# Optimization experiments

Hardware: AMD Instinct MI355X
Metric: run time of the kernel (lower is better)

## Reference

```python
import jax, jax.numpy as jnp
import numpy as np

B, T, D = 2, 2048, 1024
NH = 16
HD = D // NH


def setup_inputs() -> dict:
    key = jax.random.key(0)
    ks = jax.random.split(key, 5)
    s = 0.02
    return {
        "x": jax.random.normal(ks[0], (B, T, D), dtype=jnp.float32),
        "Wq": jax.random.normal(ks[1], (D, D), dtype=jnp.float32) * s,
        "Wk": jax.random.normal(ks[2], (D, D), dtype=jnp.float32) * s,
        "Wv": jax.random.normal(ks[3], (D, D), dtype=jnp.float32) * s,
        "Wo": jax.random.normal(ks[4], (D, D), dtype=jnp.float32) * s,
        "bo": jnp.zeros((D,), dtype=jnp.float32),
    }


def reference(x, Wq, Wk, Wv, Wo, bo):
    b, t, _ = x.shape
    scale = HD ** -0.5
    # torch Linear: y = x @ W^T
    q = (x @ Wq.T).reshape(b, t, NH, HD)
    k = (x @ Wk.T).reshape(b, t, NH, HD)
    v = (x @ Wv.T).reshape(b, t, NH, HD)
    # scores: [b, nh, t, t]
    s = jnp.einsum("bqhd,bkhd->bhqk", q, k) * scale
    causal = jnp.tril(jnp.ones((t, t), dtype=bool))
    s = jnp.where(causal, s, -jnp.inf)
    p = jax.nn.softmax(s, axis=-1)
    o = jnp.einsum("bhqk,bkhd->bqhd", p, v).reshape(b, t, D)
    return o @ Wo.T + bo
```

## Files before the change

kernel.cpp:

```cpp
#include <hip/hip_runtime.h>


typedef __bf16 bf16x8 __attribute__((ext_vector_type(8)));
typedef float f32x4 __attribute__((ext_vector_type(4)));
typedef unsigned short ushortx8 __attribute__((ext_vector_type(8)));
typedef unsigned short ushortx4 __attribute__((ext_vector_type(4)));

#define T_SEQ 2048
#define NHEAD 16
#define HDIM 64
#define DMODEL 1024

__device__ inline unsigned short f2bf(float f) {
  unsigned int u = __builtin_bit_cast(unsigned int, f);
  unsigned int r = (u + 0x7fffu + ((u >> 16) & 1u)) >> 16;
  return (unsigned short)r;
}

__device__ inline void gl16(const unsigned short* g, unsigned short* l) {
  __builtin_amdgcn_global_load_lds(
      (const __attribute__((address_space(1))) unsigned int*)g,
      (__attribute__((address_space(3))) unsigned int*)l, 16, 0, 0);
}

__global__ void cast_all(const float* __restrict__ x, const float* __restrict__ w0,
                         const float* __restrict__ w1, const float* __restrict__ w2,
                         const float* __restrict__ w3, unsigned short* __restrict__ out) {
  const int NX = 2 * T_SEQ * DMODEL;
  int i = (blockIdx.x * 256 + threadIdx.x) * 4;
  const float* src;
  int off;
  if (i < NX) {
    src = x; off = i;
  } else {
    const int j = i - NX;
    const int sel = j >> 20;
    off = j & ((1 << 20) - 1);
    src = sel == 0 ? w0 : sel == 1 ? w1 : sel == 2 ? w2 : w3;
  }
  float4 v = *reinterpret_cast<const float4*>(src + off);
  ushortx4 o;
  o[0] = f2bf(v.x); o[1] = f2bf(v.y); o[2] = f2bf(v.z); o[3] = f2bf(v.w);
  *reinterpret_cast<ushortx4*>(out + i) = o;
}

__device__ __forceinline__ void gemm_core(
    const unsigned short* __restrict__ A, const unsigned short* __restrict__ Bw,
    int K, int m0, int n0, f32x4 acc[4][4]) {
  __shared__ unsigned short As[4096];
  __shared__ unsigned short Bs[4096];
  const int tid = threadIdx.x;
  const int lane = tid & 63, wid = tid >> 6;
  const int wr = wid >> 1, wc = wid & 1;
  const int lr = lane & 15, lg = lane >> 4;
  const int srow = tid >> 2;
  const int scs = ((tid & 3) ^ (srow & 3)) * 8;
  const unsigned short* ga0 = A + (size_t)(m0 + srow) * K + scs;
  const unsigned short* gb0 = Bw + (size_t)(n0 + srow) * K + scs;
  unsigned short* la0 = As + tid * 8;
  unsigned short* lb0 = Bs + tid * 8;
  const int rca = (lg ^ (lr & 3)) * 8;

  for (int k0 = 0; k0 < K; k0 += 32) {
    __syncthreads();
    gl16(ga0 + k0, la0);
    gl16(ga0 + (size_t)64 * K + k0, la0 + 2048);
    gl16(gb0 + k0, lb0);
    gl16(gb0 + (size_t)64 * K + k0, lb0 + 2048);
    __syncthreads();

    bf16x8 af[4], bfr[4];
#pragma unroll
    for (int t = 0; t < 4; ++t) {
      af[t]  = *reinterpret_cast<const bf16x8*>(&As[(wr * 64 + t * 16 + lr) * 32 + rca]);
      bfr[t] = *reinterpret_cast<const bf16x8*>(&Bs[(wc * 64 + t * 16 + lr) * 32 + rca]);
    }
#pragma unroll
    for (int mi = 0; mi < 4; ++mi)
#pragma unroll
      for (int ni = 0; ni < 4; ++ni)
        acc[mi][ni] = __builtin_amdgcn_mfma_f32_16x16x32_bf16(af[mi], bfr[ni], acc[mi][ni], 0, 0, 0);
  }
}

__global__ __launch_bounds__(256) void gemm_qkv(
    const unsigned short* __restrict__ xb, const unsigned short* __restrict__ Wall,
    unsigned short* __restrict__ Qb, unsigned short* __restrict__ Kb,
    unsigned short* __restrict__ Vtb) {
  const int z = blockIdx.y;
  const int bid = blockIdx.x;
  int m0, n0;
  const unsigned short* A;
  const unsigned short* Bw;
  if (z < 2) {
    n0 = (bid & 7) * 128; m0 = (bid >> 3) * 128;
    A = xb; Bw = Wall + (size_t)z * (DMODEL * DMODEL);
  } else {
    m0 = (bid & 7) * 128; n0 = (bid >> 3) * 128;
    A = Wall + (size_t)2 * (DMODEL * DMODEL); Bw = xb;
  }
  f32x4 acc[4][4] = {};
  gemm_core(A, Bw, DMODEL, m0, n0, acc);

  const int tid = threadIdx.x, lane = tid & 63, wid = tid >> 6;
  const int wr = wid >> 1, wc = wid & 1, lr = lane & 15, lg = lane >> 4;
  const int mb = m0 + wr * 64, nb = n0 + wc * 64;
  const float scale = z == 0 ? 0.125f * 1.44269504089f : 1.0f;
#pragma unroll
  for (int mi = 0; mi < 4; ++mi)
#pragma unroll
    for (int ni = 0; ni < 4; ++ni) {
      const int col = nb + ni * 16 + lr;
#pragma unroll
      for (int j = 0; j < 4; ++j) {
        const int row = mb + mi * 16 + lg * 4 + j;
        const float v = acc[mi][ni][j] * scale;
        if (z < 2) {
          const int b = row >> 11, t = row & (T_SEQ - 1);
          const int h = col >> 6, d = col & (HDIM - 1);
          unsigned short* out = z == 0 ? Qb : Kb;
          out[(((size_t)(b * NHEAD + h) * T_SEQ + t) << 6) + d] = f2bf(v);
        } else {
          const int h = row >> 6, d = row & (HDIM - 1);
          const int b = col >> 11, t = col & (T_SEQ - 1);
          Vtb[(((size_t)(b * NHEAD + h) * HDIM + d) << 11) + t] = f2bf(v);
        }
      }
    }
}

__global__ __launch_bounds__(256) void gemm_proj(
    const unsigned short* __restrict__ Ob, const unsigned short* __restrict__ Wob,
    float* __restrict__ out, const float* __restrict__ bias) {
  const int m0 = blockIdx.y * 128, n0 = blockIdx.x * 128;
  f32x4 acc[4][4] = {};
  gemm_core(Ob, Wob, DMODEL, m0, n0, acc);

  const int tid = threadIdx.x, lane = tid & 63, wid = tid >> 6;
  const int wr = wid >> 1, wc = wid & 1, lr = lane & 15, lg = lane >> 4;
  const int mb = m0 + wr * 64, nb = n0 + wc * 64;
#pragma unroll
  for (int mi = 0; mi < 4; ++mi)
#pragma unroll
    for (int ni = 0; ni < 4; ++ni) {
      const int col = nb + ni * 16 + lr;
      const float bv = bias[col];
#pragma unroll
      for (int j = 0; j < 4; ++j) {
        const int row = mb + mi * 16 + lg * 4 + j;
        out[(size_t)row * DMODEL + col] = acc[mi][ni][j] + bv;
      }
    }
}

__global__ __launch_bounds__(256, 4) void flash_attn(
    const unsigned short* __restrict__ Q, const unsigned short* __restrict__ Kg,
    const unsigned short* __restrict__ Vt, unsigned short* __restrict__ O) {
  __shared__ unsigned short Ks[3][4096];
  __shared__ unsigned short Vs[3][4096];
  const int tid = threadIdx.x, lane = tid & 63, wid = tid >> 6;
  const int lr = lane & 15, lg = lane >> 4;
  const int bid = blockIdx.x;
  const int bh = (bid & 7) * 4 + ((bid >> 3) & 3);
  const int qt = 31 - (bid >> 5);
  const int qg = qt * 64 + wid * 16;
  const size_t base = (size_t)bh * (T_SEQ * HDIM);
  const int q = qg + lr;

  bf16x8 qf[2];
#pragma unroll
  for (int h = 0; h < 2; ++h)
    qf[h] = *reinterpret_cast<const bf16x8*>(Q + base + (size_t)(qg + lr) * HDIM + h * 32 + lg * 8);
  asm volatile("s_waitcnt vmcnt(0)" ::: "memory");

  const int srow = tid >> 3;
  const int schk = ((tid & 7) ^ (srow & 7)) * 8;
  const unsigned short* kst = Kg + base + (size_t)srow * HDIM + schk;
  const unsigned short* vst = Vt + base + (size_t)srow * T_SEQ + schk;

#define STAGE(buf, kt_)                                              \
  do {                                                               \
    const int kb_ = (kt_) * 64;                                      \
    gl16(kst + (size_t)kb_ * HDIM, &Ks[buf][tid * 8]);               \
    gl16(kst + (size_t)(kb_ + 32) * HDIM, &Ks[buf][2048 + tid * 8]); \
    gl16(vst + kb_, &Vs[buf][tid * 8]);                              \
    gl16(vst + 32 * T_SEQ + kb_, &Vs[buf][2048 + tid * 8]);          \
  } while (0)

  int koff[4][2];
#pragma unroll
  for (int c = 0; c < 4; ++c)
#pragma unroll
    for (int h = 0; h < 2; ++h)
      koff[c][h] = (c * 16 + lr) * 64 + (((h * 4 + lg) ^ (lr & 7)) * 8);
  int voff[4][2][2];
#pragma unroll
  for (int dt = 0; dt < 4; ++dt)
#pragma unroll
    for (int ks = 0; ks < 2; ++ks) {
      const int g0 = (ks * 4 + (lg >> 1)) ^ (lr & 7);
      const int g1 = (ks * 4 + 2 + (lg >> 1)) ^ (lr & 7);
      voff[dt][ks][0] = (dt * 16 + lr) * 64 + g0 * 8 + (lg & 1) * 4;
      voff[dt][ks][1] = (dt * 16 + lr) * 64 + g1 * 8 + (lg & 1) * 4;
    }

  float mrun = -INFINITY, lrun = 0.f;
  f32x4 acc[4] = {};
  const int nt = qt + 1;

  STAGE(0, 0);
  STAGE(1, 1);
  int cb = 0;

  for (int kt = 0; kt < nt; ++kt) {
    const int ahead = qt - kt;
    if (ahead >= 2) {
      int nb2 = cb + 2; if (nb2 >= 3) nb2 -= 3;
      STAGE(nb2, kt + 2);
      asm volatile("s_waitcnt vmcnt(8)" ::: "memory");
    } else if (ahead == 1) {
      asm volatile("s_waitcnt vmcnt(4)" ::: "memory");
    } else {
      asm volatile("s_waitcnt vmcnt(0)" ::: "memory");
    }
    __builtin_amdgcn_s_barrier();
    asm volatile("" ::: "memory");

    const int kb = kt * 64;
    f32x4 s[4] = {};
    bf16x8 kf[4][2];
#pragma unroll
    for (int c = 0; c < 4; ++c)
#pragma unroll
      for (int h = 0; h < 2; ++h)
        kf[c][h] = *reinterpret_cast<const bf16x8*>(&Ks[cb][koff[c][h]]);
    __builtin_amdgcn_s_setprio(1);
#pragma unroll
    for (int c = 0; c < 4; ++c)
#pragma unroll
      for (int h = 0; h < 2; ++h)
        s[c] = __builtin_amdgcn_mfma_f32_16x16x32_bf16(kf[c][h], qf[h], s[c], 0, 0, 0);
    __builtin_amdgcn_s_setprio(0);

    if (kt == qt) {
#pragma unroll
      for (int c = 0; c < 4; ++c)
#pragma unroll
        for (int j = 0; j < 4; ++j) {
          const int k = kb + c * 16 + lg * 4 + j;
          if (k > q) s[c][j] = -INFINITY;
        }
    }
    float tm = -INFINITY;
#pragma unroll
    for (int c = 0; c < 4; ++c)
#pragma unroll
      for (int j = 0; j < 4; ++j) tm = fmaxf(tm, s[c][j]);
    tm = fmaxf(tm, __shfl_xor(tm, 16, 64));
    tm = fmaxf(tm, __shfl_xor(tm, 32, 64));
    if (!__all(tm <= mrun + 8.f)) {
      const float mnew = fmaxf(mrun, tm);
      const float fac = exp2f(mrun - mnew);
      lrun *= fac;
#pragma unroll
      for (int dt = 0; dt < 4; ++dt)
#pragma unroll
        for (int j = 0; j < 4; ++j) acc[dt][j] *= fac;
      mrun = mnew;
    }
    float tsum = 0.f;
#pragma unroll
    for (int c = 0; c < 4; ++c)
#pragma unroll
      for (int j = 0; j < 4; ++j) {
        const float p = exp2f(s[c][j] - mrun);
        s[c][j] = p;
        tsum += p;
      }
    tsum += __shfl_xor(tsum, 16, 64);
    tsum += __shfl_xor(tsum, 32, 64);
    lrun += tsum;

    bf16x8 pb[2];
#pragma unroll
    for (int ks = 0; ks < 2; ++ks) {
      bf16x8 t8;
#pragma unroll
      for (int e = 0; e < 8; ++e) t8[e] = (__bf16)s[ks * 2 + (e >> 2)][e & 3];
      pb[ks] = t8;
    }
    __builtin_amdgcn_s_setprio(1);
#pragma unroll
    for (int dt = 0; dt < 4; ++dt) {
#pragma unroll
      for (int ks = 0; ks < 2; ++ks) {
        uint2 vlo = *reinterpret_cast<const uint2*>(&Vs[cb][voff[dt][ks][0]]);
        uint2 vhi = *reinterpret_cast<const uint2*>(&Vs[cb][voff[dt][ks][1]]);
        uint4 u;
        u.x = vlo.x; u.y = vlo.y; u.z = vhi.x; u.w = vhi.y;
        bf16x8 vf = __builtin_bit_cast(bf16x8, u);
        acc[dt] = __builtin_amdgcn_mfma_f32_16x16x32_bf16(vf, pb[ks], acc[dt], 0, 0, 0);
      }
    }
    __builtin_amdgcn_s_setprio(0);

    asm volatile("" ::: "memory");
    __builtin_amdgcn_s_barrier();
    ++cb; if (cb >= 3) cb -= 3;
  }
#undef STAGE

  const int b = bh >> 4, h = bh & (NHEAD - 1);
  const float inv = 1.0f / lrun;
  unsigned short* orow = O + (((size_t)(b * T_SEQ + q)) << 10) + h * HDIM + lg * 4;
#pragma unroll
  for (int dt = 0; dt < 4; ++dt) {
    ushortx4 o4;
#pragma unroll
    for (int j = 0; j < 4; ++j) o4[j] = f2bf(acc[dt][j] * inv);
    *reinterpret_cast<ushortx4*>(orow + dt * 16) = o4;
  }
}

extern "C" void kernel_launch(void* const* d_in, const int* in_sizes, int n_in,
                              void* d_out, int out_size, void* d_ws, size_t ws_size,
                              hipStream_t stream) {
  const float* x  = (const float*)d_in[0];
  const float* Wq = (const float*)d_in[1];
  const float* Wk = (const float*)d_in[2];
  const float* Wv = (const float*)d_in[3];
  const float* Wo = (const float*)d_in[4];
  const float* bo = (const float*)d_in[5];
  float* out = (float*)d_out;

  const int M = 2 * T_SEQ;
  const int NXD = DMODEL * DMODEL;
  const int NX = M * DMODEL;

  unsigned short* ws = (unsigned short*)d_ws;
  unsigned short* xb  = ws;
  unsigned short* Wqb = xb + NX;
  unsigned short* Wob = Wqb + 3 * (size_t)NXD;
  unsigned short* Qb  = Wqb + 4 * (size_t)NXD;
  unsigned short* Kbf = Qb + NX;
  unsigned short* Vtb = Kbf + NX;
  unsigned short* Ob  = Vtb + NX;

  cast_all<<<(NX + 4 * NXD) / 1024, 256, 0, stream>>>(x, Wq, Wk, Wv, Wo, xb);

  dim3 gq(256, 3);
  gemm_qkv<<<gq, 256, 0, stream>>>(xb, Wqb, Qb, Kbf, Vtb);

  flash_attn<<<1024, 256, 0, stream>>>(Qb, Kbf, Vtb, Ob);

  dim3 gg(DMODEL / 128, M / 128);
  gemm_proj<<<gg, 256, 0, stream>>>(Ob, Wob, out, bo);
}
```

Before: 117.8 us.

## Load K directly into registers and double-buffer V in LDS

K tiles are no longer staged through LDS. Each wave loads its K fragments straight from global memory into registers, prefetching the next tile into a second register set. V drops from a 3-deep to a 2-deep LDS ring with a single barrier per iteration, and the launch-bounds occupancy hint falls from 4 to 3. This removes the K LDS traffic and shrinks shared memory, but raises register pressure and makes every wave fetch K from global memory itself, with less prefetch depth.

```diff
diff --git a/kernel.cpp b/kernel.cpp
--- a/kernel.cpp
+++ b/kernel.cpp
@@ -153,11 +153,10 @@
     }
 }
 
-__global__ __launch_bounds__(256, 4) void flash_attn(
+__global__ __launch_bounds__(256, 3) void flash_attn(
     const unsigned short* __restrict__ Q, const unsigned short* __restrict__ Kg,
     const unsigned short* __restrict__ Vt, unsigned short* __restrict__ O) {
-  __shared__ unsigned short Ks[3][4096];
-  __shared__ unsigned short Vs[3][4096];
+  __shared__ unsigned short Vs[2][4096];
   const int tid = threadIdx.x, lane = tid & 63, wid = tid >> 6;
   const int lr = lane & 15, lg = lane >> 4;
   const int bid = blockIdx.x;
@@ -171,28 +170,27 @@
 #pragma unroll
   for (int h = 0; h < 2; ++h)
     qf[h] = *reinterpret_cast<const bf16x8*>(Q + base + (size_t)(qg + lr) * HDIM + h * 32 + lg * 8);
-  asm volatile("s_waitcnt vmcnt(0)" ::: "memory");
 
   const int srow = tid >> 3;
   const int schk = ((tid & 7) ^ (srow & 7)) * 8;
-  const unsigned short* kst = Kg + base + (size_t)srow * HDIM + schk;
   const unsigned short* vst = Vt + base + (size_t)srow * T_SEQ + schk;
 
-#define STAGE(buf, kt_)                                              \
-  do {                                                               \
-    const int kb_ = (kt_) * 64;                                      \
-    gl16(kst + (size_t)kb_ * HDIM, &Ks[buf][tid * 8]);               \
-    gl16(kst + (size_t)(kb_ + 32) * HDIM, &Ks[buf][2048 + tid * 8]); \
-    gl16(vst + kb_, &Vs[buf][tid * 8]);                              \
-    gl16(vst + 32 * T_SEQ + kb_, &Vs[buf][2048 + tid * 8]);          \
+#define STAGE(buf, kt_)                                      \
+  do {                                                       \
+    const int kb_ = (kt_) * 64;                              \
+    gl16(vst + kb_, &Vs[buf][tid * 8]);                      \
+    gl16(vst + 32 * T_SEQ + kb_, &Vs[buf][2048 + tid * 8]);  \
   } while (0)
 
-  int koff[4][2];
-#pragma unroll
-  for (int c = 0; c < 4; ++c)
-#pragma unroll
-    for (int h = 0; h < 2; ++h)
-      koff[c][h] = (c * 16 + lr) * 64 + (((h * 4 + lg) ^ (lr & 7)) * 8);
+  const unsigned short* kp = Kg + base + (size_t)lr * HDIM + lg * 8;
+#define KLOAD(dst, kt_)                                                      \
+  do {                                                                       \
+    const unsigned short* kpp = kp + (size_t)(kt_) * 64 * HDIM;              \
+    _Pragma("unroll") for (int c = 0; c < 4; ++c)                            \
+      _Pragma("unroll") for (int h = 0; h < 2; ++h)                          \
+        dst[c][h] = *reinterpret_cast<const bf16x8*>(kpp + c * 16 * HDIM + h * 32); \
+  } while (0)
+
   int voff[4][2][2];
 #pragma unroll
   for (int dt = 0; dt < 4; ++dt)
@@ -208,38 +206,27 @@
   f32x4 acc[4] = {};
   const int nt = qt + 1;
 
+  bf16x8 kfA[4][2], kfB[4][2];
   STAGE(0, 0);
-  STAGE(1, 1);
-  int cb = 0;
+  KLOAD(kfA, 0);
 
   for (int kt = 0; kt < nt; ++kt) {
-    const int ahead = qt - kt;
-    if (ahead >= 2) {
-      int nb2 = cb + 2; if (nb2 >= 3) nb2 -= 3;
-      STAGE(nb2, kt + 2);
-      asm volatile("s_waitcnt vmcnt(8)" ::: "memory");
-    } else if (ahead == 1) {
-      asm volatile("s_waitcnt vmcnt(4)" ::: "memory");
-    } else {
-      asm volatile("s_waitcnt vmcnt(0)" ::: "memory");
-    }
+    asm volatile("s_waitcnt vmcnt(0)" ::: "memory");
     __builtin_amdgcn_s_barrier();
     asm volatile("" ::: "memory");
+    if (kt + 1 < nt) {
+      STAGE((kt + 1) & 1, kt + 1);
+      KLOAD(kfB, kt + 1);
+    }
 
     const int kb = kt * 64;
     f32x4 s[4] = {};
-    bf16x8 kf[4][2];
+    __builtin_amdgcn_s_setprio(1);
 #pragma unroll
     for (int c = 0; c < 4; ++c)
 #pragma unroll
       for (int h = 0; h < 2; ++h)
-        kf[c][h] = *reinterpret_cast<const bf16x8*>(&Ks[cb][koff[c][h]]);
-    __builtin_amdgcn_s_setprio(1);
-#pragma unroll
-    for (int c = 0; c < 4; ++c)
-#pragma unroll
-      for (int h = 0; h < 2; ++h)
-        s[c] = __builtin_amdgcn_mfma_f32_16x16x32_bf16(kf[c][h], qf[h], s[c], 0, 0, 0);
+        s[c] = __builtin_amdgcn_mfma_f32_16x16x32_bf16(kfA[c][h], qf[h], s[c], 0, 0, 0);
     __builtin_amdgcn_s_setprio(0);
 
     if (kt == qt) {
@@ -294,8 +281,8 @@
     for (int dt = 0; dt < 4; ++dt) {
 #pragma unroll
       for (int ks = 0; ks < 2; ++ks) {
-        uint2 vlo = *reinterpret_cast<const uint2*>(&Vs[cb][voff[dt][ks][0]]);
-        uint2 vhi = *reinterpret_cast<const uint2*>(&Vs[cb][voff[dt][ks][1]]);
+        uint2 vlo = *reinterpret_cast<const uint2*>(&Vs[kt & 1][voff[dt][ks][0]]);
+        uint2 vhi = *reinterpret_cast<const uint2*>(&Vs[kt & 1][voff[dt][ks][1]]);
         uint4 u;
         u.x = vlo.x; u.y = vlo.y; u.z = vhi.x; u.w = vhi.y;
         bf16x8 vf = __builtin_bit_cast(bf16x8, u);
@@ -304,11 +291,15 @@
     }
     __builtin_amdgcn_s_setprio(0);
 
-    asm volatile("" ::: "memory");
-    __builtin_amdgcn_s_barrier();
-    ++cb; if (cb >= 3) cb -= 3;
+    if (kt + 1 < nt) {
+#pragma unroll
+      for (int c = 0; c < 4; ++c)
+#pragma unroll
+        for (int h = 0; h < 2; ++h) kfA[c][h] = kfB[c][h];
+    }
   }
 #undef STAGE
+#undef KLOAD
 
   const int b = bh >> 4, h = bh & (NHEAD - 1);
   const float inv = 1.0f / lrun;
```

After: 150.1 us. 27.4% more time.

## Double-buffer GEMM LDS tiles and switch attention to two-stage prefetch

Applied to the files above, without the earlier changes.

The GEMM core now holds two LDS buffers and prefetches the next K tile while MFMAs run on the current one. Before, each K step had a full load-and-wait between two barriers. The flash attention kernel goes from a three-buffer, two-ahead pipeline to a two-buffer, one-ahead scheme with one vmcnt(0)+barrier per iteration. This cuts LDS use and may raise occupancy, but leaves less time to hide load latency in attention. The GEMM also doubles its LDS footprint.

```diff
diff --git a/kernel.cpp b/kernel.cpp
--- a/kernel.cpp
+++ b/kernel.cpp
@@ -47,8 +47,8 @@
 __device__ __forceinline__ void gemm_core(
     const unsigned short* __restrict__ A, const unsigned short* __restrict__ Bw,
     int K, int m0, int n0, f32x4 acc[4][4]) {
-  __shared__ unsigned short As[4096];
-  __shared__ unsigned short Bs[4096];
+  __shared__ unsigned short As[2][4096];
+  __shared__ unsigned short Bs[2][4096];
   const int tid = threadIdx.x;
   const int lane = tid & 63, wid = tid >> 6;
   const int wr = wid >> 1, wc = wid & 1;
@@ -57,30 +57,42 @@
   const int scs = ((tid & 3) ^ (srow & 3)) * 8;
   const unsigned short* ga0 = A + (size_t)(m0 + srow) * K + scs;
   const unsigned short* gb0 = Bw + (size_t)(n0 + srow) * K + scs;
-  unsigned short* la0 = As + tid * 8;
-  unsigned short* lb0 = Bs + tid * 8;
   const int rca = (lg ^ (lr & 3)) * 8;
 
+#define STAGE_G(buf, k0_)                                            \
+  do {                                                               \
+    gl16(ga0 + (k0_), &As[buf][tid * 8]);                            \
+    gl16(ga0 + (size_t)64 * K + (k0_), &As[buf][2048 + tid * 8]);    \
+    gl16(gb0 + (k0_), &Bs[buf][tid * 8]);                            \
+    gl16(gb0 + (size_t)64 * K + (k0_), &Bs[buf][2048 + tid * 8]);    \
+  } while (0)
+
+  STAGE_G(0, 0);
+  asm volatile("s_waitcnt vmcnt(0)" ::: "memory");
+  __builtin_amdgcn_s_barrier();
+  asm volatile("" ::: "memory");
+
   for (int k0 = 0; k0 < K; k0 += 32) {
-    __syncthreads();
-    gl16(ga0 + k0, la0);
-    gl16(ga0 + (size_t)64 * K + k0, la0 + 2048);
-    gl16(gb0 + k0, lb0);
-    gl16(gb0 + (size_t)64 * K + k0, lb0 + 2048);
-    __syncthreads();
+    const int cb = (k0 >> 5) & 1;
+    if (k0 + 32 < K) STAGE_G(cb ^ 1, k0 + 32);
 
     bf16x8 af[4], bfr[4];
 #pragma unroll
     for (int t = 0; t < 4; ++t) {
-      af[t]  = *reinterpret_cast<const bf16x8*>(&As[(wr * 64 + t * 16 + lr) * 32 + rca]);
-      bfr[t] = *reinterpret_cast<const bf16x8*>(&Bs[(wc * 64 + t * 16 + lr) * 32 + rca]);
+      af[t]  = *reinterpret_cast<const bf16x8*>(&As[cb][(wr * 64 + t * 16 + lr) * 32 + rca]);
+      bfr[t] = *reinterpret_cast<const bf16x8*>(&Bs[cb][(wc * 64 + t * 16 + lr) * 32 + rca]);
     }
 #pragma unroll
     for (int mi = 0; mi < 4; ++mi)
 #pragma unroll
       for (int ni = 0; ni < 4; ++ni)
         acc[mi][ni] = __builtin_amdgcn_mfma_f32_16x16x32_bf16(af[mi], bfr[ni], acc[mi][ni], 0, 0, 0);
-  }
+
+    asm volatile("s_waitcnt vmcnt(0)" ::: "memory");
+    __builtin_amdgcn_s_barrier();
+    asm volatile("" ::: "memory");
+  }
+#undef STAGE_G
 }
 
 __global__ __launch_bounds__(256) void gemm_qkv(
@@ -156,8 +168,8 @@
 __global__ __launch_bounds__(256, 4) void flash_attn(
     const unsigned short* __restrict__ Q, const unsigned short* __restrict__ Kg,
     const unsigned short* __restrict__ Vt, unsigned short* __restrict__ O) {
-  __shared__ unsigned short Ks[3][4096];
-  __shared__ unsigned short Vs[3][4096];
+  __shared__ unsigned short Ks[2][4096];
+  __shared__ unsigned short Vs[2][4096];
   const int tid = threadIdx.x, lane = tid & 63, wid = tid >> 6;
   const int lr = lane & 15, lg = lane >> 4;
   const int bid = blockIdx.x;
@@ -171,7 +183,6 @@
 #pragma unroll
   for (int h = 0; h < 2; ++h)
     qf[h] = *reinterpret_cast<const bf16x8*>(Q + base + (size_t)(qg + lr) * HDIM + h * 32 + lg * 8);
-  asm volatile("s_waitcnt vmcnt(0)" ::: "memory");
 
   const int srow = tid >> 3;
   const int schk = ((tid & 7) ^ (srow & 7)) * 8;
@@ -209,22 +220,13 @@
   const int nt = qt + 1;
 
   STAGE(0, 0);
-  STAGE(1, 1);
-  int cb = 0;
+  asm volatile("s_waitcnt vmcnt(0)" ::: "memory");
+  __builtin_amdgcn_s_barrier();
+  asm volatile("" ::: "memory");
 
   for (int kt = 0; kt < nt; ++kt) {
-    const int ahead = qt - kt;
-    if (ahead >= 2) {
-      int nb2 = cb + 2; if (nb2 >= 3) nb2 -= 3;
-      STAGE(nb2, kt + 2);
-      asm volatile("s_waitcnt vmcnt(8)" ::: "memory");
-    } else if (ahead == 1) {
-      asm volatile("s_waitcnt vmcnt(4)" ::: "memory");
-    } else {
-      asm volatile("s_waitcnt vmcnt(0)" ::: "memory");
-    }
-    __builtin_amdgcn_s_barrier();
-    asm volatile("" ::: "memory");
+    const int cb = kt & 1;
+    if (kt + 1 < nt) STAGE(cb ^ 1, kt + 1);
 
     const int kb = kt * 64;
     f32x4 s[4] = {};
@@ -304,9 +306,9 @@
     }
     __builtin_amdgcn_s_setprio(0);
 
+    asm volatile("s_waitcnt vmcnt(0)" ::: "memory");
+    __builtin_amdgcn_s_barrier();
     asm volatile("" ::: "memory");
-    __builtin_amdgcn_s_barrier();
-    ++cb; if (cb >= 3) cb -= 3;
   }
 #undef STAGE
 
```

Result: no change. 118.4 us (+0.5%).
